# Performance work log

Measured on AMD Instinct MI355X. Metric: run time of the kernel, lower is better.

Reference implementation:

```python
import jax, jax.numpy as jnp
import numpy as np

DIM = 1024
AUX = 3
B, S = 32, 1024
ENC_D = DIM * AUX  # 3072


def setup_inputs() -> dict:
    key = jax.random.key(0)
    ks = jax.random.split(key, 5)
    sc1 = 1.0 / np.sqrt(DIM * (AUX + 1))
    sc3 = 1.0 / np.sqrt(ENC_D)
    return {
        "hidden_state": jax.random.normal(ks[0], (B, DIM), jnp.float32),
        "encoder_outputs": jax.random.normal(ks[1], (B, S, ENC_D), jnp.float32),
        "W1": jax.random.normal(ks[2], (DIM, DIM * (AUX + 1)), jnp.float32) * sc1,
        "b1": jnp.zeros((DIM,), jnp.float32),
        "w2": jax.random.normal(ks[3], (1, DIM), jnp.float32) * (1.0 / np.sqrt(DIM)),
        "W3": jax.random.normal(ks[4], (DIM, ENC_D), jnp.float32) * sc3,
        "b3": jnp.zeros((DIM,), jnp.float32),
    }


def reference(hidden_state, encoder_outputs, W1, b1, w2, W3, b3):
    # hidden_state: (B, dim); encoder_outputs: (B, S, dim*aux)
    Bsz, Slen, _ = encoder_outputs.shape
    h = jnp.broadcast_to(hidden_state[:, None, :], (Bsz, Slen, hidden_state.shape[-1]))
    inputs = jnp.concatenate([encoder_outputs, h], axis=2)  # (B, S, dim*(aux+1))
    # score MLP: tanh(linear1) -> linear2 (no bias)
    hidden = jnp.tanh(jnp.einsum('bsf,df->bsd', inputs, W1) + b1)  # (B, S, dim)
    e = jnp.einsum('bsd,od->bso', hidden, w2)[..., 0]  # (B, S)
    alpha = jax.nn.softmax(e, axis=1)
    context = jnp.einsum('bs,bsf->bf', alpha, encoder_outputs)  # (B, dim*aux)
    return jnp.einsum('bf,df->bd', context, W3) + b3  # (B, dim)
```

## Files before the change

### kernel.cpp

```cpp
#include <hip/hip_runtime.h>
#include <hip/hip_bf16.h>


typedef float          fx4 __attribute__((ext_vector_type(4)));
typedef short          sv8 __attribute__((ext_vector_type(8)));
typedef unsigned short uv4 __attribute__((ext_vector_type(4)));
typedef unsigned int   ui4 __attribute__((ext_vector_type(4)));

__device__ __forceinline__ unsigned short f2bf(float x) {
  unsigned u = __float_as_uint(x);
  return (unsigned short)((u + 0x7FFFu + ((u >> 16) & 1u)) >> 16);
}
__device__ __forceinline__ unsigned cvtpk(float lo, float hi) {
  unsigned r;
  asm("v_cvt_pk_bf16_f32 %0, %1, %2" : "=v"(r) : "v"(lo), "v"(hi));
  return r;
}
__device__ __forceinline__ ui4 pack8(fx4 a, fx4 b) {
  ui4 v;
  v[0] = cvtpk(a[0], a[1]); v[1] = cvtpk(a[2], a[3]);
  v[2] = cvtpk(b[0], b[1]); v[3] = cvtpk(b[2], b[3]);
  return v;
}

#define GLD(srcp, dstp)                                               \
  __builtin_amdgcn_global_load_lds(                                   \
      (const __attribute__((address_space(1))) void*)(srcp),          \
      (__attribute__((address_space(3))) void*)(dstp), 16, 0, 0)

__global__ void convw1_kernel(const float* __restrict__ W1, unsigned short* __restrict__ W1a) {
  int id = blockIdx.x * 256 + threadIdx.x;
  int d = id / 768, fi = id - d * 768;
  fx4 v = ((const fx4*)W1)[d * 1024 + fi];
  uv4 r; r[0] = f2bf(v[0]); r[1] = f2bf(v[1]); r[2] = f2bf(v[2]); r[3] = f2bf(v[3]);
  ((uv4*)W1a)[d * 768 + fi] = r;
}

__global__ void convenc_kernel(const float* __restrict__ enc, unsigned short* __restrict__ ebf) {
  int id = blockIdx.x * 256 + threadIdx.x;
  fx4 a = ((const fx4*)enc)[2 * id];
  fx4 b = ((const fx4*)enc)[2 * id + 1];
  ((ui4*)ebf)[id] = pack8(a, b);
}

__global__ void hbias_kernel(const float* __restrict__ hs, const float* __restrict__ W1,
                             const float* __restrict__ b1, float* __restrict__ hb) {
  int idx = (blockIdx.x << 2) + (threadIdx.x >> 6);
  int lane = threadIdx.x & 63;
  int b = idx >> 10, d = idx & 1023;
  const fx4* hv = (const fx4*)hs;
  const fx4* wv = (const fx4*)W1;
  float s = 0.f;
#pragma unroll
  for (int i = 0; i < 4; ++i) {
    int k4 = lane + (i << 6);
    fx4 h = hv[(b << 8) + k4];
    fx4 w = wv[d * 1024 + 768 + k4];
    s += h[0] * w[0] + h[1] * w[1] + h[2] * w[2] + h[3] * w[3];
  }
#pragma unroll
  for (int off = 32; off; off >>= 1) s += __shfl_xor(s, off);
  if (lane == 0) hb[idx] = s + b1[d];
}

__global__ __launch_bounds__(512, 2)
void gemm8(const unsigned short* __restrict__ Ag,
           const unsigned short* __restrict__ Bg,
           const float* __restrict__ hb,
           const float* __restrict__ w2,
           float* __restrict__ pe) {
  __shared__ __align__(16) unsigned short Ab[3][16384];
  __shared__ __align__(16) unsigned short Bb[2][16384];

  const int t = threadIdx.x, lane = t & 63, wid = t >> 6;
  const int wm = wid >> 2, wn = wid & 3;

  const int bid = blockIdx.x;
  const int lg = ((bid & 7) << 6) | (bid >> 3);
  const int mt = lg >> 2, nt = lg & 3;
  const int row0 = mt << 8, col0 = nt << 8;

  const int l3 = lane >> 3, l7 = lane & 7;
  const unsigned short* asrc = Ag + (size_t)(row0 + wid * 32 + l3) * 3072 + ((l7 ^ l3) << 3);
  const unsigned short* bsrc = Bg + (size_t)(col0 + wid * 32 + l3) * 3072 + ((l7 ^ l3) << 3);
  const int dstb = wid << 11;

  const int r15 = lane & 15, qv = lane >> 4;
  const int aB = (wm * 128 + r15) << 6;
  const int bB = (wn * 64 + r15) << 6;
  const int s0 = (qv ^ (r15 & 7)) << 3;
  const int s1 = ((qv + 4) ^ (r15 & 7)) << 3;

  fx4 acc[8][4] = {};
  sv8 bfv[4];

#define ST_B(BN, kt, g) GLD(bsrc + (g) * 24576 + (kt) * 64, &Bb[BN][dstb + ((g) << 9)])
#define ST_A(AN, kt, g) GLD(asrc + (g) * 24576 + (kt) * 64, &Ab[AN][dstb + ((g) << 9)])

#define PHASE(AB, BBUF, MH, KH, ISSUE)                                \
  { sv8 af[4];                                                        \
    const int sx = (KH) ? s1 : s0;                                    \
    _Pragma("unroll")                                                 \
    for (int mi = 0; mi < 4; ++mi)                                    \
      af[mi] = *(const sv8*)&Ab[AB][aB + (((MH) * 64 + mi * 16) << 6) + sx]; \
    if ((MH) == 0) {                                                  \
      _Pragma("unroll")                                               \
      for (int ni = 0; ni < 4; ++ni)                                  \
        bfv[ni] = *(const sv8*)&Bb[BBUF][bB + ((ni * 16) << 6) + sx]; \
    }                                                                 \
    ISSUE                                                             \
    __builtin_amdgcn_s_setprio(1);                                    \
    _Pragma("unroll")                                                 \
    for (int mi = 0; mi < 4; ++mi)                                    \
      _Pragma("unroll")                                               \
      for (int ni = 0; ni < 4; ++ni)                                  \
        acc[(MH) * 4 + mi][ni] = __builtin_amdgcn_mfma_f32_16x16x32_bf16( \
            af[mi], bfv[ni], acc[(MH) * 4 + mi][ni], 0, 0, 0);        \
    __builtin_amdgcn_s_setprio(0);                                    \
  }

#define TILE(kt, AB, BBUF, BN, AN)                                    \
  PHASE(AB, BBUF, 0, 0, { if ((kt) < 47) { ST_B(BN, (kt) + 1, 0); ST_B(BN, (kt) + 1, 1); } }) \
  PHASE(AB, BBUF, 1, 0, { if ((kt) < 47) { ST_B(BN, (kt) + 1, 2); ST_B(BN, (kt) + 1, 3); } }) \
  PHASE(AB, BBUF, 0, 1, { if ((kt) < 46) { ST_A(AN, (kt) + 2, 0); ST_A(AN, (kt) + 2, 1); } }) \
  PHASE(AB, BBUF, 1, 1, { if ((kt) < 46) { ST_A(AN, (kt) + 2, 2); ST_A(AN, (kt) + 2, 3); } }) \
  if ((kt) < 46)       { asm volatile("s_waitcnt vmcnt(4)" ::: "memory"); } \
  else if ((kt) == 46) { asm volatile("s_waitcnt vmcnt(0)" ::: "memory"); } \
  __builtin_amdgcn_s_barrier();

  ST_B(0, 0, 0); ST_B(0, 0, 1); ST_B(0, 0, 2); ST_B(0, 0, 3);
  ST_A(0, 0, 0); ST_A(0, 0, 1); ST_A(0, 0, 2); ST_A(0, 0, 3);
  ST_A(1, 1, 0); ST_A(1, 1, 1); ST_A(1, 1, 2); ST_A(1, 1, 3);
  asm volatile("s_waitcnt vmcnt(4)" ::: "memory");
  __builtin_amdgcn_s_barrier();

  for (int it = 0; it < 8; ++it) {
    const int k6 = it * 6;
    TILE(k6 + 0, 0, 0, 1, 2)
    TILE(k6 + 1, 1, 1, 0, 0)
    TILE(k6 + 2, 2, 0, 1, 1)
    TILE(k6 + 3, 0, 1, 0, 2)
    TILE(k6 + 4, 1, 0, 1, 0)
    TILE(k6 + 5, 2, 1, 0, 1)
  }

  const int b = row0 >> 10;
  float w2v[4], hbv[4];
#pragma unroll
  for (int ni = 0; ni < 4; ++ni) {
    int c = col0 + wn * 64 + ni * 16 + r15;
    w2v[ni] = w2[c];
    hbv[ni] = hb[(b << 10) + c];
  }
#pragma unroll
  for (int mi = 0; mi < 8; ++mi) {
#pragma unroll
    for (int j = 0; j < 4; ++j) {
      float pz = 0.f;
#pragma unroll
      for (int ni = 0; ni < 4; ++ni)
        pz += tanhf(acc[mi][ni][j] + hbv[ni]) * w2v[ni];
      pz += __shfl_xor(pz, 1); pz += __shfl_xor(pz, 2);
      pz += __shfl_xor(pz, 4); pz += __shfl_xor(pz, 8);
      if (r15 == 0) {
        int row = row0 + wm * 128 + mi * 16 + (qv << 2) + j;
        pe[(row << 4) + (nt << 2) + wn] = pz;
      }
    }
  }
#undef ST_A
#undef ST_B
#undef PHASE
#undef TILE
}

__global__ __launch_bounds__(512, 2)
void gemm2(const float* __restrict__ enc,
           const unsigned short* __restrict__ W1a,
           const float* __restrict__ hb,
           const float* __restrict__ w2,
           float* __restrict__ pe) {
  __shared__ __align__(16) unsigned short As[2][10240];
  __shared__ __align__(16) unsigned short Bs[2][8192];
  const int t = threadIdx.x;
  const int lane = t & 63, wid = t >> 6;
  const int wm = wid >> 2, wn = wid & 3;
  const int bid = blockIdx.x;
  const int lg = ((bid & 7) << 6) | (bid >> 3);
  const int mt = lg >> 2, ntile = lg & 3;
  const int row0 = mt << 8;
  const int col0 = ntile << 8;
  const fx4* encv = (const fx4*)enc;
  const int ar = t >> 1, ah = t & 1;
  const int agb = (row0 + ar) * 768 + ah * 4;
  const int awb = ar * 40 + ah * 16;
  const int l3 = lane >> 3, l7 = lane & 7;
  const int pre = l7 ^ l3;
  const unsigned short* bsrc0 =
      W1a + (size_t)(col0 + wid * 32 + 2 * l3 + (pre >> 2)) * 3072 + (pre & 3) * 8;
  const unsigned short* bsrc1 = bsrc0 + (size_t)16 * 3072;
  const int bdst0 = (wid * 16) * 64;
  const int bdst1 = (wid * 16 + 8) * 64;
  const int r15 = lane & 15, qv = lane >> 4;
  const int aro = (wm * 128 + r15) * 40 + qv * 8;
  const int cb = wn * 64 + r15;
  const int bro = (cb >> 1) * 64 + (((((cb & 1) << 2) + qv) ^ ((cb >> 1) & 7)) << 3);
  fx4 acc[8][4] = {};
  fx4 pa[2][4];
#define A_LOAD(s, kt) { _Pragma("unroll") for (int j = 0; j < 4; ++j) pa[s][j] = encv[agb + (kt) * 8 + j]; }
#define A_WRITE(s, buf) { *(ui4*)&As[buf][awb] = pack8(pa[s][0], pa[s][1]); \
                          *(ui4*)&As[buf][awb + 8] = pack8(pa[s][2], pa[s][3]); }
#define B_ISSUE(buf, kt) { GLD(bsrc0 + (kt) * 32, &Bs[buf][bdst0]); \
                           GLD(bsrc1 + (kt) * 32, &Bs[buf][bdst1]); }
#define COMPUTE(p)                                                    \
  { sv8 af[8], bfv[4];                                                \
    _Pragma("unroll")                                                 \
    for (int mi = 0; mi < 8; ++mi) af[mi] = *(const sv8*)&As[p][aro + mi * 640]; \
    _Pragma("unroll")                                                 \
    for (int ni = 0; ni < 4; ++ni) bfv[ni] = *(const sv8*)&Bs[p][bro + ni * 512]; \
    _Pragma("unroll")                                                 \
    for (int mi = 0; mi < 8; ++mi)                                    \
      _Pragma("unroll")                                               \
      for (int ni = 0; ni < 4; ++ni)                                  \
        acc[mi][ni] = __builtin_amdgcn_mfma_f32_16x16x32_bf16(af[mi], bfv[ni], acc[mi][ni], 0, 0, 0); }
#define ITER(kt, p)                                                   \
  { COMPUTE(p)                                                        \
    if ((kt) < 95) { A_WRITE(p ^ 1, p ^ 1) }                          \
    if ((kt) < 93) { A_LOAD(p ^ 1, (kt) + 3) }                        \
    __builtin_amdgcn_s_barrier();                                     \
    if ((kt) < 94) {                                                  \
      B_ISSUE(p, (kt) + 2)                                            \
      asm volatile("s_waitcnt vmcnt(6)" ::: "memory");                \
    } else if ((kt) == 94) {                                          \
      asm volatile("s_waitcnt vmcnt(0)" ::: "memory");                \
    }                                                                 \
    asm volatile("s_waitcnt lgkmcnt(0)" ::: "memory");                \
    __builtin_amdgcn_s_barrier(); }
  A_LOAD(0, 0)
  A_LOAD(1, 1)
  B_ISSUE(0, 0)
  A_WRITE(0, 0)
  B_ISSUE(1, 1)
  A_LOAD(0, 2)
  asm volatile("s_waitcnt vmcnt(6)" ::: "memory");
  asm volatile("s_waitcnt lgkmcnt(0)" ::: "memory");
  __builtin_amdgcn_s_barrier();
  for (int kt2 = 0; kt2 < 48; ++kt2) {
    const int kt = kt2 * 2;
    ITER(kt, 0)
    ITER(kt + 1, 1)
  }
  const int b = row0 >> 10;
  float w2v[4], hbv[4];
#pragma unroll
  for (int ni = 0; ni < 4; ++ni) {
    int c = col0 + wn * 64 + ni * 16 + r15;
    w2v[ni] = w2[c];
    hbv[ni] = hb[(b << 10) + c];
  }
#pragma unroll
  for (int mi = 0; mi < 8; ++mi) {
#pragma unroll
    for (int j = 0; j < 4; ++j) {
      float pz = 0.f;
#pragma unroll
      for (int ni = 0; ni < 4; ++ni)
        pz += tanhf(acc[mi][ni][j] + hbv[ni]) * w2v[ni];
      pz += __shfl_xor(pz, 1); pz += __shfl_xor(pz, 2);
      pz += __shfl_xor(pz, 4); pz += __shfl_xor(pz, 8);
      if (r15 == 0) {
        int row = row0 + wm * 128 + mi * 16 + (qv << 2) + j;
        pe[(row << 4) + (ntile << 2) + wn] = pz;
      }
    }
  }
#undef A_LOAD
#undef A_WRITE
#undef B_ISSUE
#undef COMPUTE
#undef ITER
}

__global__ void softmax_kernel(const float* __restrict__ pe, float* __restrict__ alpha) {
  int b = blockIdx.x, t = threadIdx.x;
  int lane = t & 63, wid = t >> 6;
  float ev[4];
#pragma unroll
  for (int r = 0; r < 4; ++r) {
    int s = t + r * 256;
    const float* p = pe + ((b << 10) + s) * 16;
    float sum = 0.f;
#pragma unroll
    for (int i = 0; i < 16; ++i) sum += p[i];
    ev[r] = sum;
  }
  float m = fmaxf(fmaxf(ev[0], ev[1]), fmaxf(ev[2], ev[3]));
#pragma unroll
  for (int off = 32; off; off >>= 1) m = fmaxf(m, __shfl_xor(m, off));
  __shared__ float red[8];
  if (lane == 0) red[wid] = m;
  __syncthreads();
  m = fmaxf(fmaxf(red[0], red[1]), fmaxf(red[2], red[3]));
  float p4[4], ls = 0.f;
#pragma unroll
  for (int r = 0; r < 4; ++r) { p4[r] = expf(ev[r] - m); ls += p4[r]; }
#pragma unroll
  for (int off = 32; off; off >>= 1) ls += __shfl_xor(ls, off);
  if (lane == 0) red[4 + wid] = ls;
  __syncthreads();
  float inv = 1.0f / (red[4] + red[5] + red[6] + red[7]);
#pragma unroll
  for (int r = 0; r < 4; ++r) alpha[(b << 10) + t + r * 256] = p4[r] * inv;
}

__global__ void ctxpart_bf_kernel(const unsigned short* __restrict__ ebf,
                                  const float* __restrict__ alpha,
                                  float* __restrict__ part) {
  int bid = blockIdx.x, b = bid >> 4, sc = bid & 15;
  int t = threadIdx.x;
  __shared__ float sal[64];
  if (t < 64) sal[t] = alpha[(b << 10) + (sc << 6) + t];
  __syncthreads();
  const ui4* ev = (const ui4*)ebf;
  float a8[8] = {};
  int base = ((b << 10) + (sc << 6)) * 384;
  for (int si = 0; si < 64; ++si) {
    float a = sal[si];
    ui4 v = ev[base + si * 384 + t];
#pragma unroll
    for (int j = 0; j < 4; ++j) {
      unsigned u = v[j];
      a8[2 * j]     += a * __uint_as_float(u << 16);
      a8[2 * j + 1] += a * __uint_as_float(u & 0xFFFF0000u);
    }
  }
  fx4* pp = (fx4*)part;
  int pb = ((b << 4) + sc) * 768 + t * 2;
  fx4 o0 = {a8[0], a8[1], a8[2], a8[3]};
  fx4 o1 = {a8[4], a8[5], a8[6], a8[7]};
  pp[pb] = o0; pp[pb + 1] = o1;
}

__global__ void ctxpart_kernel(const float* __restrict__ enc, const float* __restrict__ alpha,
                               float* __restrict__ part) {
  int bid = blockIdx.x, b = bid >> 4, sc = bid & 15;
  int t = threadIdx.x;
  __shared__ float sal[64];
  if (t < 64) sal[t] = alpha[(b << 10) + (sc << 6) + t];
  __syncthreads();
  const fx4* ev = (const fx4*)enc;
  fx4 a0 = {}, a1 = {}, a2 = {};
  int base = ((b << 10) + (sc << 6)) * 768;
  for (int si = 0; si < 64; ++si) {
    float a = sal[si];
    const fx4* rp = ev + base + si * 768;
    a0 += a * rp[t];
    a1 += a * rp[256 + t];
    a2 += a * rp[512 + t];
  }
  fx4* pp = (fx4*)part;
  int pb = ((b << 4) + sc) * 768;
  pp[pb + t] = a0; pp[pb + 256 + t] = a1; pp[pb + 512 + t] = a2;
}

__global__ void ctxreduce_kernel(const float* __restrict__ part, float* __restrict__ ctx) {
  int j = blockIdx.x * 256 + threadIdx.x;
  int b = j / 768, fi = j - b * 768;
  const fx4* pp = (const fx4*)part;
  fx4 s = {};
#pragma unroll
  for (int i = 0; i < 16; ++i) s += pp[((b << 4) + i) * 768 + fi];
  ((fx4*)ctx)[b * 768 + fi] = s;
}

__global__ void final_kernel(const float* __restrict__ ctx, const float* __restrict__ W3,
                             const float* __restrict__ b3, float* __restrict__ out) {
  int idx = (blockIdx.x << 2) + (threadIdx.x >> 6);
  int lane = threadIdx.x & 63;
  int b = idx >> 10, d = idx & 1023;
  const fx4* cv = (const fx4*)ctx;
  const fx4* wv = (const fx4*)W3;
  float s = 0.f;
#pragma unroll
  for (int i = 0; i < 12; ++i) {
    int f4 = lane + (i << 6);
    fx4 c = cv[b * 768 + f4];
    fx4 w = wv[d * 768 + f4];
    s += c[0] * w[0] + c[1] * w[1] + c[2] * w[2] + c[3] * w[3];
  }
#pragma unroll
  for (int off = 32; off; off >>= 1) s += __shfl_xor(s, off);
  if (lane == 0) out[idx] = s + b3[d];
}

extern "C" void kernel_launch(void* const* d_in, const int* in_sizes, int n_in,
                              void* d_out, int out_size, void* d_ws, size_t ws_size,
                              hipStream_t stream) {
  const float* hs  = (const float*)d_in[0];
  const float* enc = (const float*)d_in[1];
  const float* W1  = (const float*)d_in[2];
  const float* b1  = (const float*)d_in[3];
  const float* w2  = (const float*)d_in[4];
  const float* W3  = (const float*)d_in[5];
  const float* b3  = (const float*)d_in[6];
  float* out = (float*)d_out;
  char* ws = (char*)d_ws;

  const size_t NEED_A = 216662016ULL;

  if (ws_size >= NEED_A) {
    unsigned short* ebf = (unsigned short*)(ws);
    unsigned short* W1a = (unsigned short*)(ws + 201326592);
    float* pe    = (float*)(ws + 207618048);
    float* alpha = (float*)(ws + 209715200);
    float* hb    = (float*)(ws + 209846272);
    float* ctx   = (float*)(ws + 209977344);
    float* part  = (float*)(ws + 210370560);

    convw1_kernel<<<3072, 256, 0, stream>>>(W1, W1a);
    convenc_kernel<<<49152, 256, 0, stream>>>(enc, ebf);
    hbias_kernel<<<8192, 256, 0, stream>>>(hs, W1, b1, hb);
    gemm8<<<512, 512, 0, stream>>>(ebf, W1a, hb, w2, pe);
    softmax_kernel<<<32, 256, 0, stream>>>(pe, alpha);
    ctxpart_bf_kernel<<<512, 384, 0, stream>>>(ebf, alpha, part);
    ctxreduce_kernel<<<96, 256, 0, stream>>>(part, ctx);
    final_kernel<<<8192, 256, 0, stream>>>(ctx, W3, b3, out);
  } else {
    unsigned short* W1a = (unsigned short*)(ws);
    float* pe    = (float*)(ws + 6291456);
    float* alpha = (float*)(ws + 8388608);
    float* hb    = (float*)(ws + 8519680);
    float* ctx   = (float*)(ws + 8650752);
    float* part  = (float*)(ws + 9043968);

    convw1_kernel<<<3072, 256, 0, stream>>>(W1, W1a);
    hbias_kernel<<<8192, 256, 0, stream>>>(hs, W1, b1, hb);
    gemm2<<<512, 512, 0, stream>>>(enc, W1a, hb, w2, pe);
    softmax_kernel<<<32, 256, 0, stream>>>(pe, alpha);
    ctxpart_kernel<<<512, 256, 0, stream>>>(enc, alpha, part);
    ctxreduce_kernel<<<96, 256, 0, stream>>>(part, ctx);
    final_kernel<<<8192, 256, 0, stream>>>(ctx, W3, b3, out);
  }
}
```

Before: 410.0 us.

## Load W1 fragments directly into registers and shrink A buffering to double

In gemm8 the B operand (W1 in bf16) is no longer staged through LDS. Each wave now loads its MFMA B fragments straight from global memory into a double-buffered register array. A staging drops from a triple buffer to a double buffer, with a full vmcnt/lgkmcnt drain before every barrier. The aim is to cut LDS traffic and footprint, at the cost of more VGPRs, redundant global loads of B across the two wm waves, and a shallower prefetch pipeline.

```diff
diff --git a/kernel.cpp b/kernel.cpp
--- a/kernel.cpp
+++ b/kernel.cpp
@@ -69,8 +69,7 @@
            const float* __restrict__ hb,
            const float* __restrict__ w2,
            float* __restrict__ pe) {
-  __shared__ __align__(16) unsigned short Ab[3][16384];
-  __shared__ __align__(16) unsigned short Bb[2][16384];
+  __shared__ __align__(16) unsigned short Ab[2][16384];
 
   const int t = threadIdx.x, lane = t & 63, wid = t >> 6;
   const int wm = wid >> 2, wn = wid & 3;
@@ -82,66 +81,66 @@
 
   const int l3 = lane >> 3, l7 = lane & 7;
   const unsigned short* asrc = Ag + (size_t)(row0 + wid * 32 + l3) * 3072 + ((l7 ^ l3) << 3);
-  const unsigned short* bsrc = Bg + (size_t)(col0 + wid * 32 + l3) * 3072 + ((l7 ^ l3) << 3);
   const int dstb = wid << 11;
 
   const int r15 = lane & 15, qv = lane >> 4;
   const int aB = (wm * 128 + r15) << 6;
-  const int bB = (wn * 64 + r15) << 6;
   const int s0 = (qv ^ (r15 & 7)) << 3;
   const int s1 = ((qv + 4) ^ (r15 & 7)) << 3;
 
+  const unsigned short* bp0 = Bg + (size_t)(col0 + wn * 64 + 0 * 16 + r15) * 3072 + qv * 8;
+  const unsigned short* bp1 = Bg + (size_t)(col0 + wn * 64 + 1 * 16 + r15) * 3072 + qv * 8;
+  const unsigned short* bp2 = Bg + (size_t)(col0 + wn * 64 + 2 * 16 + r15) * 3072 + qv * 8;
+  const unsigned short* bp3 = Bg + (size_t)(col0 + wn * 64 + 3 * 16 + r15) * 3072 + qv * 8;
+
   fx4 acc[8][4] = {};
-  sv8 bfv[4];
-
-#define ST_B(BN, kt, g) GLD(bsrc + (g) * 24576 + (kt) * 64, &Bb[BN][dstb + ((g) << 9)])
+  sv8 bfv[2][8];
+
 #define ST_A(AN, kt, g) GLD(asrc + (g) * 24576 + (kt) * 64, &Ab[AN][dstb + ((g) << 9)])
-
-#define PHASE(AB, BBUF, MH, KH, ISSUE)                                \
+#define LDB(P, kh)                                                    \
+  { bfv[P][(kh) * 4 + 0] = *(const sv8*)(bp0 + (kh) * 32);            \
+    bfv[P][(kh) * 4 + 1] = *(const sv8*)(bp1 + (kh) * 32);            \
+    bfv[P][(kh) * 4 + 2] = *(const sv8*)(bp2 + (kh) * 32);            \
+    bfv[P][(kh) * 4 + 3] = *(const sv8*)(bp3 + (kh) * 32); }
+#define BADV  { bp0 += 64; bp1 += 64; bp2 += 64; bp3 += 64; }
+
+#define PHASE(P, MH, KH)                                              \
   { sv8 af[4];                                                        \
     const int sx = (KH) ? s1 : s0;                                    \
     _Pragma("unroll")                                                 \
     for (int mi = 0; mi < 4; ++mi)                                    \
-      af[mi] = *(const sv8*)&Ab[AB][aB + (((MH) * 64 + mi * 16) << 6) + sx]; \
-    if ((MH) == 0) {                                                  \
-      _Pragma("unroll")                                               \
-      for (int ni = 0; ni < 4; ++ni)                                  \
-        bfv[ni] = *(const sv8*)&Bb[BBUF][bB + ((ni * 16) << 6) + sx]; \
-    }                                                                 \
-    ISSUE                                                             \
+      af[mi] = *(const sv8*)&Ab[P][aB + (((MH) * 64 + mi * 16) << 6) + sx]; \
     __builtin_amdgcn_s_setprio(1);                                    \
     _Pragma("unroll")                                                 \
     for (int mi = 0; mi < 4; ++mi)                                    \
       _Pragma("unroll")                                               \
       for (int ni = 0; ni < 4; ++ni)                                  \
         acc[(MH) * 4 + mi][ni] = __builtin_amdgcn_mfma_f32_16x16x32_bf16( \
-            af[mi], bfv[ni], acc[(MH) * 4 + mi][ni], 0, 0, 0);        \
+            af[mi], bfv[P][(KH) * 4 + ni], acc[(MH) * 4 + mi][ni], 0, 0, 0); \
     __builtin_amdgcn_s_setprio(0);                                    \
   }
 
-#define TILE(kt, AB, BBUF, BN, AN)                                    \
-  PHASE(AB, BBUF, 0, 0, { if ((kt) < 47) { ST_B(BN, (kt) + 1, 0); ST_B(BN, (kt) + 1, 1); } }) \
-  PHASE(AB, BBUF, 1, 0, { if ((kt) < 47) { ST_B(BN, (kt) + 1, 2); ST_B(BN, (kt) + 1, 3); } }) \
-  PHASE(AB, BBUF, 0, 1, { if ((kt) < 46) { ST_A(AN, (kt) + 2, 0); ST_A(AN, (kt) + 2, 1); } }) \
-  PHASE(AB, BBUF, 1, 1, { if ((kt) < 46) { ST_A(AN, (kt) + 2, 2); ST_A(AN, (kt) + 2, 3); } }) \
-  if ((kt) < 46)       { asm volatile("s_waitcnt vmcnt(4)" ::: "memory"); } \
-  else if ((kt) == 46) { asm volatile("s_waitcnt vmcnt(0)" ::: "memory"); } \
+#define TILE(kt, P)                                                   \
+  { if ((kt) < 47) { ST_A(P ^ 1, (kt) + 1, 0); ST_A(P ^ 1, (kt) + 1, 1); \
+                     ST_A(P ^ 1, (kt) + 1, 2); ST_A(P ^ 1, (kt) + 1, 3); } \
+    PHASE(P, 0, 0)                                                    \
+    PHASE(P, 1, 0)                                                    \
+    if ((kt) < 47) { LDB(P ^ 1, 0) }                                  \
+    PHASE(P, 0, 1)                                                    \
+    PHASE(P, 1, 1)                                                    \
+    if ((kt) < 47) { LDB(P ^ 1, 1) BADV }                             \
+    asm volatile("s_waitcnt lgkmcnt(0)" ::: "memory");                \
+    asm volatile("s_waitcnt vmcnt(0)" ::: "memory");                  \
+    __builtin_amdgcn_s_barrier(); }
+
+  ST_A(0, 0, 0); ST_A(0, 0, 1); ST_A(0, 0, 2); ST_A(0, 0, 3);
+  LDB(0, 0) LDB(0, 1) BADV
+  asm volatile("s_waitcnt vmcnt(0)" ::: "memory");
   __builtin_amdgcn_s_barrier();
 
-  ST_B(0, 0, 0); ST_B(0, 0, 1); ST_B(0, 0, 2); ST_B(0, 0, 3);
-  ST_A(0, 0, 0); ST_A(0, 0, 1); ST_A(0, 0, 2); ST_A(0, 0, 3);
-  ST_A(1, 1, 0); ST_A(1, 1, 1); ST_A(1, 1, 2); ST_A(1, 1, 3);
-  asm volatile("s_waitcnt vmcnt(4)" ::: "memory");
-  __builtin_amdgcn_s_barrier();
-
-  for (int it = 0; it < 8; ++it) {
-    const int k6 = it * 6;
-    TILE(k6 + 0, 0, 0, 1, 2)
-    TILE(k6 + 1, 1, 1, 0, 0)
-    TILE(k6 + 2, 2, 0, 1, 1)
-    TILE(k6 + 3, 0, 1, 0, 2)
-    TILE(k6 + 4, 1, 0, 1, 0)
-    TILE(k6 + 5, 2, 1, 0, 1)
+  for (int it = 0; it < 24; ++it) {
+    TILE(2 * it, 0)
+    TILE(2 * it + 1, 1)
   }
 
   const int b = row0 >> 10;
@@ -169,7 +168,8 @@
     }
   }
 #undef ST_A
-#undef ST_B
+#undef LDB
+#undef BADV
 #undef PHASE
 #undef TILE
 }
```

Measured after the change: 503.1 us. +22.7%, slower.
